# Optimization experiments

Measured on AMD Instinct MI355X. Metric: run time of the kernel, lower is better.

Reference implementation:

```python
import jax, jax.numpy as jnp
import numpy as np

D_MODEL = 1024
NUM_HEADS = 16
DEPTH = D_MODEL // NUM_HEADS


def setup_inputs() -> dict:
    key = jax.random.key(0)
    ks = jax.random.split(key, 9)
    B, S = 2, 2048
    scale = 1.0 / np.sqrt(D_MODEL)
    x = jax.random.normal(ks[0], (B, S, D_MODEL), dtype=jnp.float32)
    wq = jax.random.normal(ks[1], (D_MODEL, D_MODEL), dtype=jnp.float32) * scale
    bq = jax.random.normal(ks[2], (D_MODEL,), dtype=jnp.float32) * 0.01
    wk = jax.random.normal(ks[3], (D_MODEL, D_MODEL), dtype=jnp.float32) * scale
    bk = jax.random.normal(ks[4], (D_MODEL,), dtype=jnp.float32) * 0.01
    wv = jax.random.normal(ks[5], (D_MODEL, D_MODEL), dtype=jnp.float32) * scale
    bv = jax.random.normal(ks[6], (D_MODEL,), dtype=jnp.float32) * 0.01
    wo = jax.random.normal(ks[7], (D_MODEL, D_MODEL), dtype=jnp.float32) * scale
    bo = jax.random.normal(ks[8], (D_MODEL,), dtype=jnp.float32) * 0.01
    return {"x": x, "wq": wq, "bq": bq, "wk": wk, "bk": bk,
            "wv": wv, "bv": bv, "wo": wo, "bo": bo}


def reference(x, wq, bq, wk, bk, wv, bv, wo, bo):
    B, S, _ = x.shape
    def split_heads(t):  # [B,S,D] -> [B,H,S,depth]
        return t.reshape(B, S, NUM_HEADS, DEPTH).transpose(0, 2, 1, 3)
    q = split_heads(x @ wq + bq)
    k = split_heads(x @ wk + bk)
    v = split_heads(x @ wv + bv)
    # scaled dot-product attention, full [B,H,S,S] scores as in the original
    logits = jnp.einsum('bhqd,bhkd->bhqk', q, k) / jnp.sqrt(
        jnp.asarray(DEPTH, dtype=jnp.float32))
    attn = jax.nn.softmax(logits, axis=-1)
    out = jnp.einsum('bhqk,bhkd->bhqd', attn, v)
    out = out.transpose(0, 2, 1, 3).reshape(B, S, D_MODEL)
    return out @ wo + bo
```

## Files before the change

### kernel.cpp

```cpp
#include <hip/hip_runtime.h>


#define S_LEN 2048
#define DM 1024
#define MROWS 4096
#define QSCALE 0.1803368801111244f

typedef unsigned short u16;
typedef unsigned int u32;
typedef __attribute__((ext_vector_type(8))) short short8;
typedef __attribute__((ext_vector_type(4))) float f32x4;
typedef __attribute__((ext_vector_type(4))) unsigned short u16x4;
typedef __attribute__((ext_vector_type(2))) unsigned int u32x2;

__device__ inline u16 f2bf(float f) {
    u32 u = __float_as_uint(f);
    u = u + 0x7fffu + ((u >> 16) & 1u);
    return (u16)(u >> 16);
}
__device__ inline void gld_lds16(const u16* g, u16* l) {
    __builtin_amdgcn_global_load_lds(
        (const __attribute__((address_space(1))) void*)g,
        (__attribute__((address_space(3))) void*)l, 16, 0, 0);
}
__device__ inline f32x4 mfma16(short8 a, short8 b, f32x4 c) {
    return __builtin_amdgcn_mfma_f32_16x16x32_bf16(a, b, c, 0, 0, 0);
}

__global__ void prep_all(const float* __restrict__ x, u16* __restrict__ xb,
                         const float* __restrict__ wq, const float* __restrict__ wk,
                         const float* __restrict__ wv, const float* __restrict__ wo,
                         const float* __restrict__ bq, const float* __restrict__ bk,
                         const float* __restrict__ bv, const float* __restrict__ bo,
                         u16* __restrict__ wallT, u16* __restrict__ woT,
                         float* __restrict__ biasAll, float* __restrict__ biasO) {
    const int t = threadIdx.x;
    if (blockIdx.x < 2048) {
        const size_t i8 = ((size_t)blockIdx.x * 256 + t) * 8;
        const f32x4 a = ((const f32x4*)x)[i8 / 4];
        const f32x4 b = ((const f32x4*)x)[i8 / 4 + 1];
        u16 o[8];
#pragma unroll
        for (int i = 0; i < 4; i++) { o[i] = f2bf(a[i]); o[4 + i] = f2bf(b[i]); }
        *(short8*)(xb + i8) = *(const short8*)o;
        return;
    }
    const int bid = blockIdx.x - 2048;
    if (bid == 1024) {
#pragma unroll
        for (int i = 0; i < 4; i++) {
            const int idx = i * 256 + t;
            biasAll[idx]        = bq[idx] * QSCALE;
            biasAll[1024 + idx] = bk[idx];
            biasAll[2048 + idx] = bv[idx];
            biasO[idx]          = bo[idx];
        }
        return;
    }
    __shared__ float lds[64][65];
    const int m  = bid >> 8;
    const int tk = (bid >> 4) & 15;
    const int tn = bid & 15;
    const float* src = (m == 0) ? wq : (m == 1) ? wk : (m == 2) ? wv : wo;
    const float scale = (m == 0) ? QSCALE : 1.0f;
    const int r4 = t >> 6, c = t & 63;
#pragma unroll
    for (int i = 0; i < 16; i++) {
        const int k = tk * 64 + i * 4 + r4;
        lds[i * 4 + r4][c] = src[(size_t)k * 1024 + tn * 64 + c];
    }
    __syncthreads();
#pragma unroll
    for (int i = 0; i < 16; i++) {
        const int n = tn * 64 + i * 4 + r4;
        const int k = tk * 64 + c;
        const u16 v = f2bf(lds[c][i * 4 + r4] * scale);
        if (m < 3) wallT[((size_t)m * 1024 + n) * 1024 + k] = v;
        else       woT[(size_t)n * 1024 + k] = v;
    }
}

__global__ __launch_bounds__(256, 3)
void gemm_qkv(const u16* __restrict__ A, const u16* __restrict__ Bt,
              const float* __restrict__ bias, u16* __restrict__ Cq,
              u16* __restrict__ Ck, u16* __restrict__ Cv,
              const int K, const int N) {
    __shared__ __align__(16) u16 As[128 * 32];
    __shared__ __align__(16) u16 Bs[128 * 32];
    __shared__ __align__(16) u16 Ct[128 * 136];
    const int tid = threadIdx.x;
    const int w = tid >> 6, lane = tid & 63;
    const int wm = w >> 1, wn = w & 1;
    const int l16 = lane & 15, quad = lane >> 4;
    const int tm = blockIdx.x * 128;
    const int tn = blockIdx.y * 128;
    const int region = tn >> 10;

    const int sr = w * 16 + (lane >> 2);
    const int sc = (lane & 3) * 8;
    const u16* ag0 = A + (size_t)(tm + sr) * K + sc;
    const u16* ag1 = A + (size_t)(tm + sr + 64) * K + sc;
    const u16* bg0 = Bt + (size_t)(tn + sr) * K + sc;
    const u16* bg1 = Bt + (size_t)(tn + sr + 64) * K + sc;
    u16* al = As + w * 512;
    u16* bl = Bs + w * 512;

    f32x4 acc[4][4];
#pragma unroll
    for (int i = 0; i < 4; i++)
#pragma unroll
        for (int j = 0; j < 4; j++) acc[i][j] = (f32x4){0.f, 0.f, 0.f, 0.f};

    for (int kb = 0; kb < K; kb += 32) {
        __syncthreads();
        gld_lds16(ag0 + kb, al);
        gld_lds16(ag1 + kb, al + 2048);
        gld_lds16(bg0 + kb, bl);
        gld_lds16(bg1 + kb, bl + 2048);
        __syncthreads();
        short8 af[4], bfr[4];
#pragma unroll
        for (int i = 0; i < 4; i++) {
            af[i]  = *(const short8*)(As + (wm * 64 + i * 16 + l16) * 32 + quad * 8);
            bfr[i] = *(const short8*)(Bs + (wn * 64 + i * 16 + l16) * 32 + quad * 8);
        }
#pragma unroll
        for (int i = 0; i < 4; i++)
#pragma unroll
            for (int j = 0; j < 4; j++)
                acc[i][j] = mfma16(af[i], bfr[j], acc[i][j]);
    }

    if (region < 2) {
#pragma unroll
        for (int j = 0; j < 4; j++) {
            const int colL = wn * 64 + j * 16 + l16;
            const float bv = bias[tn + colL];
#pragma unroll
            for (int i = 0; i < 4; i++) {
                const int row0 = wm * 64 + i * 16 + quad * 4;
#pragma unroll
                for (int r = 0; r < 4; r++)
                    Ct[(row0 + r) * 136 + colL] = f2bf(acc[i][j][r] + bv);
            }
        }
    } else {
#pragma unroll
        for (int j = 0; j < 4; j++) {
            const int colL = wn * 64 + j * 16 + l16;
            const float bv = bias[tn + colL];
#pragma unroll
            for (int i = 0; i < 4; i++) {
                const int row0 = wm * 64 + i * 16 + quad * 4;
                u16x4 pk;
#pragma unroll
                for (int r = 0; r < 4; r++) pk[r] = f2bf(acc[i][j][r] + bv);
                *(u16x4*)(Ct + colL * 132 + row0) = pk;
            }
        }
    }
    __syncthreads();

    if (region == 0) {
#pragma unroll
        for (int p = 0; p < 8; p++) {
            const int rowL = p * 16 + (tid >> 4);
            const int c8 = (tid & 15) * 8;
            const short8 v = *(const short8*)(Ct + rowL * 136 + c8);
            *(short8*)(Cq + (size_t)(tm + rowL) * 1024 + tn + c8) = v;
        }
    } else if (region == 1) {
        const int b = tm >> 11, sBase = tm & 2047;
#pragma unroll
        for (int p = 0; p < 8; p++) {
            const int rowL = p * 16 + (tid >> 4);
            const int c8 = (tid & 15) * 8;
            const short8 v = *(const short8*)(Ct + rowL * 136 + c8);
            const int s = sBase + rowL;
            const int hd = (tn - 1024) + c8;
            const int h = hd >> 6, dd = hd & 63;
            const int chunk = ((dd >> 3) + s) & 7;
            *(short8*)(Ck + (((size_t)(b * 16 + h) * 2048 + s) << 6) + chunk * 8) = v;
        }
    } else {
        const int b = tm >> 11, tBase = (tm & 2047) >> 6;
        const int hBase = (tn >> 6) - 32;
#pragma unroll
        for (int p = 0; p < 8; p++) {
            const int cid = p * 256 + tid;
            const int q3 = cid & 7;
            const int colL = (cid >> 3) & 127;
            const int half = cid >> 10;
            const int d = colL & 63;
            const int h = hBase + (colL >> 6);
            const int c = (q3 - d) & 7;
            const int base = (c & 3) * 4 + ((c & 4) << 3);
            const u32x2 Ar = *(const u32x2*)(Ct + colL * 132 + half * 64 + base);
            const u32x2 Br = *(const u32x2*)(Ct + colL * 132 + half * 64 + base + 16);
            union { u32 u[4]; short8 s8; } o;
            o.u[0] = __builtin_amdgcn_perm(Br[0], Ar[0], 0x05040100u);
            o.u[1] = __builtin_amdgcn_perm(Br[0], Ar[0], 0x07060302u);
            o.u[2] = __builtin_amdgcn_perm(Br[1], Ar[1], 0x05040100u);
            o.u[3] = __builtin_amdgcn_perm(Br[1], Ar[1], 0x07060302u);
            *(short8*)(Cv + (((size_t)((b * 16 + h) * 32 + tBase + half)) << 12) +
                       d * 64 + q3 * 8) = o.s8;
        }
    }
}

__global__ __launch_bounds__(256, 2)
void gemm_out64(const u16* __restrict__ A, const u16* __restrict__ Bt,
                const float* __restrict__ bias, float* __restrict__ C,
                const int K, const int N) {
    __shared__ __align__(16) u16 As[64 * 32];
    __shared__ __align__(16) u16 Bs[128 * 32];
    const int tid = threadIdx.x;
    const int w = tid >> 6, lane = tid & 63;
    const int wm = w >> 1, wn = w & 1;
    const int l16 = lane & 15, quad = lane >> 4;
    const int tm = blockIdx.x * 64;
    const int tn = blockIdx.y * 128;

    const int sr = w * 16 + (lane >> 2);
    const int sc = (lane & 3) * 8;
    const u16* ag  = A + (size_t)(tm + sr) * K + sc;
    const u16* bg0 = Bt + (size_t)(tn + sr) * K + sc;
    const u16* bg1 = Bt + (size_t)(tn + sr + 64) * K + sc;
    u16* al = As + w * 512;
    u16* bl = Bs + w * 512;

    f32x4 acc[2][4];
#pragma unroll
    for (int i = 0; i < 2; i++)
#pragma unroll
        for (int j = 0; j < 4; j++) acc[i][j] = (f32x4){0.f, 0.f, 0.f, 0.f};

    for (int kb = 0; kb < K; kb += 32) {
        __syncthreads();
        gld_lds16(ag + kb, al);
        gld_lds16(bg0 + kb, bl);
        gld_lds16(bg1 + kb, bl + 2048);
        __syncthreads();
        short8 af[2], bfr[4];
#pragma unroll
        for (int i = 0; i < 2; i++)
            af[i] = *(const short8*)(As + (wm * 32 + i * 16 + l16) * 32 + quad * 8);
#pragma unroll
        for (int j = 0; j < 4; j++)
            bfr[j] = *(const short8*)(Bs + (wn * 64 + j * 16 + l16) * 32 + quad * 8);
#pragma unroll
        for (int i = 0; i < 2; i++)
#pragma unroll
            for (int j = 0; j < 4; j++)
                acc[i][j] = mfma16(af[i], bfr[j], acc[i][j]);
    }
#pragma unroll
    for (int j = 0; j < 4; j++) {
        const int col = tn + wn * 64 + j * 16 + l16;
        const float bv = bias[col];
#pragma unroll
        for (int i = 0; i < 2; i++) {
            const int row0 = tm + wm * 32 + i * 16 + quad * 4;
#pragma unroll
            for (int r = 0; r < 4; r++)
                C[(size_t)(row0 + r) * N + col] = acc[i][j][r] + bv;
        }
    }
}

__global__ __launch_bounds__(256, 2)
void flash_attn(const u16* __restrict__ Qb, const u16* __restrict__ Ktg,
                const u16* __restrict__ Vtb, u16* __restrict__ O) {
    __shared__ __align__(16) u16 Ks[4096];
    __shared__ __align__(16) u16 Vs[4096];
    const int tid = threadIdx.x;
    const int w = tid >> 6, lane = tid & 63;
    const int l16 = lane & 15, quad = lane >> 4;
    const int lid = blockIdx.x + blockIdx.y * 16;
    const int bh = lid & 31, b = bh >> 4, h = bh & 15;
    const int q0 = (lid >> 5) * 128 + w * 32;

    short8 qf[2][2];
#pragma unroll
    for (int u = 0; u < 2; u++) {
        const size_t qrow = (size_t)(b * S_LEN + q0 + u * 16 + l16) * 1024 + h * 64;
        qf[u][0] = *(const short8*)(Qb + qrow + quad * 8);
        qf[u][1] = *(const short8*)(Qb + qrow + 32 + quad * 8);
    }
    u16 ones_s[8];
#pragma unroll
    for (int i = 0; i < 8; i++) ones_s[i] = 0x3F80u;
    const short8 ones = *(const short8*)ones_s;

    const u16* kg = Ktg + ((size_t)bh << 17) + w * 1024 + lane * 8;
    const u16* vg = Vtb + ((size_t)bh << 17) + w * 1024 + lane * 8;
    u16* kl = Ks + w * 1024;
    u16* vl = Vs + w * 1024;

    const int ka0 = l16 * 64 + ((quad + l16) & 7) * 8;
    const int ka1 = l16 * 64 + ((4 + quad + l16) & 7) * 8;

    f32x4 o[2][4], osum[2];
#pragma unroll
    for (int u = 0; u < 2; u++) {
        osum[u] = (f32x4){0.f, 0.f, 0.f, 0.f};
#pragma unroll
        for (int d = 0; d < 4; d++) o[u][d] = (f32x4){0.f, 0.f, 0.f, 0.f};
    }
    const f32x4 zz = (f32x4){0.f, 0.f, 0.f, 0.f};

    for (int t = 0; t < S_LEN / 64; t++) {
        __syncthreads();
        const int off = t * 4096;
        gld_lds16(kg + off,       kl);
        gld_lds16(kg + off + 512, kl + 512);
        gld_lds16(vg + off,       vl);
        gld_lds16(vg + off + 512, vl + 512);
        __syncthreads();

        f32x4 s[2][4];
#pragma unroll
        for (int a = 0; a < 4; a++) {
            const short8 kf0 = *(const short8*)(Ks + a * 1024 + ka0);
            const short8 kf1 = *(const short8*)(Ks + a * 1024 + ka1);
#pragma unroll
            for (int u = 0; u < 2; u++) {
                s[u][a] = mfma16(kf0, qf[u][0], zz);
                s[u][a] = mfma16(kf1, qf[u][1], s[u][a]);
            }
        }
        union { u32 u[4]; short8 s8; } pu[2][2];
#pragma unroll
        for (int u = 0; u < 2; u++) {
#pragma unroll
            for (int r = 0; r < 4; r++) {
                const float e0 = __builtin_amdgcn_exp2f(s[u][0][r]);
                const float e1 = __builtin_amdgcn_exp2f(s[u][1][r]);
                const float e2 = __builtin_amdgcn_exp2f(s[u][2][r]);
                const float e3 = __builtin_amdgcn_exp2f(s[u][3][r]);
                pu[u][0].u[r] = __builtin_amdgcn_perm(
                    __float_as_uint(e1), __float_as_uint(e0), 0x07060302u);
                pu[u][1].u[r] = __builtin_amdgcn_perm(
                    __float_as_uint(e3), __float_as_uint(e2), 0x07060302u);
            }
            osum[u] = mfma16(ones, pu[u][0].s8, osum[u]);
            osum[u] = mfma16(ones, pu[u][1].s8, osum[u]);
        }
#pragma unroll
        for (int dv = 0; dv < 4; dv++) {
            const short8 vf0 = *(const short8*)(Vs + dv * 1024 + ka0);
            const short8 vf1 = *(const short8*)(Vs + dv * 1024 + ka1);
#pragma unroll
            for (int u = 0; u < 2; u++) {
                o[u][dv] = mfma16(vf0, pu[u][0].s8, o[u][dv]);
                o[u][dv] = mfma16(vf1, pu[u][1].s8, o[u][dv]);
            }
        }
    }

#pragma unroll
    for (int u = 0; u < 2; u++) {
        const float inv = 1.0f / osum[u][0];
        const size_t obase =
            (size_t)(b * S_LEN + q0 + u * 16 + l16) * DM + h * 64 + quad * 4;
#pragma unroll
        for (int d = 0; d < 4; d++) {
            u16x4 pk;
#pragma unroll
            for (int r = 0; r < 4; r++) pk[r] = f2bf(o[u][d][r] * inv);
            *(u16x4*)(O + obase + d * 16) = pk;
        }
    }
}

extern "C" void kernel_launch(void* const* d_in, const int* in_sizes, int n_in,
                              void* d_out, int out_size, void* d_ws, size_t ws_size,
                              hipStream_t stream) {
    const float* x  = (const float*)d_in[0];
    const float* wq = (const float*)d_in[1];
    const float* bq = (const float*)d_in[2];
    const float* wk = (const float*)d_in[3];
    const float* bk = (const float*)d_in[4];
    const float* wv = (const float*)d_in[5];
    const float* bv = (const float*)d_in[6];
    const float* wo = (const float*)d_in[7];
    const float* bo = (const float*)d_in[8];

    char* ws = (char*)d_ws;
    u16*   wallT   = (u16*)(ws + 64);
    u16*   woT     = (u16*)(ws + 6291520);
    float* biasAll = (float*)(ws + 8388672);
    float* biasO   = (float*)(ws + 8400960);
    u16*   xb      = (u16*)(ws + 8405056);
    u16*   Qb      = (u16*)(ws + 16793664);
    u16*   Ktg     = (u16*)(ws + 25182272);
    u16*   Vtb     = (u16*)(ws + 33570880);
    u16*   Obuf    = (u16*)(ws + 41959488);

    prep_all<<<3073, 256, 0, stream>>>(x, xb, wq, wk, wv, wo, bq, bk, bv, bo,
                                       wallT, woT, biasAll, biasO);
    gemm_qkv<<<dim3(32, 24), 256, 0, stream>>>(xb, wallT, biasAll,
                                               Qb, Ktg, Vtb, 1024, 3072);
    flash_attn<<<dim3(16, 32), 256, 0, stream>>>(Qb, Ktg, Vtb, Obuf);
    gemm_out64<<<dim3(64, 8), 256, 0, stream>>>(Obuf, woT, biasO,
                                                (float*)d_out, 1024, 1024);
}
```

Measured before the change: 177.4 us.

## Double K-tile depth in QKV GEMM with XOR-swizzled LDS and aliased epilogue buffer

Raises the QKV projection GEMM's K step from 32 to 64, which halves the number of barrier pairs per tile. Shared-memory reads now use an XOR swizzle on 16-byte chunks to avoid bank conflicts. The operand buffers and the output staging tile now share one LDS allocation, guarded by an extra barrier, so LDS use stays small enough to raise the occupancy hint from 3 to 4 blocks. The risk is higher register pressure under the tighter launch bound, and the loop still has no load/compute overlap.

After: 186.7 us. 1.05x slower.

```diff
diff --git a/kernel.cpp b/kernel.cpp
--- a/kernel.cpp
+++ b/kernel.cpp
@@ -80,14 +80,15 @@
     }
 }
 
-__global__ __launch_bounds__(256, 3)
+__global__ __launch_bounds__(256, 4)
 void gemm_qkv(const u16* __restrict__ A, const u16* __restrict__ Bt,
               const float* __restrict__ bias, u16* __restrict__ Cq,
               u16* __restrict__ Ck, u16* __restrict__ Cv,
               const int K, const int N) {
-    __shared__ __align__(16) u16 As[128 * 32];
-    __shared__ __align__(16) u16 Bs[128 * 32];
-    __shared__ __align__(16) u16 Ct[128 * 136];
+    __shared__ __align__(16) u16 SMEM[17408];
+    u16* As = SMEM;
+    u16* Bs = SMEM + 8192;
+    u16* Ct = SMEM;
     const int tid = threadIdx.x;
     const int w = tid >> 6, lane = tid & 63;
     const int wm = w >> 1, wn = w & 1;
@@ -96,14 +97,12 @@
     const int tn = blockIdx.y * 128;
     const int region = tn >> 10;
 
-    const int sr = w * 16 + (lane >> 2);
-    const int sc = (lane & 3) * 8;
-    const u16* ag0 = A + (size_t)(tm + sr) * K + sc;
-    const u16* ag1 = A + (size_t)(tm + sr + 64) * K + sc;
-    const u16* bg0 = Bt + (size_t)(tn + sr) * K + sc;
-    const u16* bg1 = Bt + (size_t)(tn + sr + 64) * K + sc;
-    u16* al = As + w * 512;
-    u16* bl = Bs + w * 512;
+    const int sr8 = lane >> 3;
+    const int sc8 = ((lane & 7) ^ sr8) * 8;
+    const u16* ag = A + (size_t)(tm + w * 32 + sr8) * K + sc8;
+    const u16* bg = Bt + (size_t)(tn + w * 32 + sr8) * K + sc8;
+    u16* al = As + w * 2048;
+    u16* bl = Bs + w * 2048;
 
     f32x4 acc[4][4];
 #pragma unroll
@@ -111,25 +110,34 @@
 #pragma unroll
         for (int j = 0; j < 4; j++) acc[i][j] = (f32x4){0.f, 0.f, 0.f, 0.f};
 
-    for (int kb = 0; kb < K; kb += 32) {
-        __syncthreads();
-        gld_lds16(ag0 + kb, al);
-        gld_lds16(ag1 + kb, al + 2048);
-        gld_lds16(bg0 + kb, bl);
-        gld_lds16(bg1 + kb, bl + 2048);
-        __syncthreads();
-        short8 af[4], bfr[4];
-#pragma unroll
-        for (int i = 0; i < 4; i++) {
-            af[i]  = *(const short8*)(As + (wm * 64 + i * 16 + l16) * 32 + quad * 8);
-            bfr[i] = *(const short8*)(Bs + (wn * 64 + i * 16 + l16) * 32 + quad * 8);
-        }
-#pragma unroll
-        for (int i = 0; i < 4; i++)
-#pragma unroll
-            for (int j = 0; j < 4; j++)
-                acc[i][j] = mfma16(af[i], bfr[j], acc[i][j]);
-    }
+    const int swz = l16 & 7;
+    for (int kb = 0; kb < K; kb += 64) {
+        __syncthreads();
+#pragma unroll
+        for (int j = 0; j < 4; j++) {
+            gld_lds16(ag + kb + (size_t)j * 8 * K, al + j * 512);
+            gld_lds16(bg + kb + (size_t)j * 8 * K, bl + j * 512);
+        }
+        __syncthreads();
+#pragma unroll
+        for (int ks = 0; ks < 2; ks++) {
+            short8 af[4], bfr[4];
+#pragma unroll
+            for (int i = 0; i < 4; i++) {
+                const int c = ks * 4 + quad;
+                af[i]  = *(const short8*)(As + (wm * 64 + i * 16 + l16) * 64 +
+                                          ((c ^ swz) * 8));
+                bfr[i] = *(const short8*)(Bs + (wn * 64 + i * 16 + l16) * 64 +
+                                          ((c ^ swz) * 8));
+            }
+#pragma unroll
+            for (int i = 0; i < 4; i++)
+#pragma unroll
+                for (int j = 0; j < 4; j++)
+                    acc[i][j] = mfma16(af[i], bfr[j], acc[i][j]);
+        }
+    }
+    __syncthreads();
 
     if (region < 2) {
 #pragma unroll
```
